# Optimization experiments

Measured on AMD Instinct MI355X. Metric: run time of the kernel, lower is better.

## Reference

```python
import jax, jax.numpy as jnp
import numpy as np

EPS = 0.1          # entropic regularization (init eps)
MAX_ITER = 20      # Sinkhorn iterations (init max_iter)
THRESH = 0.1       # convergence threshold on err (from torch source)
COS_EPS = 1e-8     # CosineSimilarity eps


def setup_inputs() -> dict:
    key = jax.random.key(0)
    kx, ky = jax.random.split(key)
    B, N, M, D = 4, 1024, 1024, 512
    x = jax.random.normal(kx, (B, N, D), dtype=jnp.float32)
    y = jax.random.normal(ky, (B, M, D), dtype=jnp.float32)
    nu = jnp.full((B, M), 1.0 / M, dtype=jnp.float32)  # target marginal
    return {"x": x, "y": y, "nu": nu}


def _cost_matrix(x, y):
    # C_ij = 1 - cos(x_i, y_j), with torch CosineSimilarity eps semantics
    dot = jnp.einsum("bnd,bmd->bnm", x, y)
    nx = jnp.linalg.norm(x, axis=-1)  # [B, N]
    ny = jnp.linalg.norm(y, axis=-1)  # [B, M]
    denom = jnp.maximum(nx[:, :, None] * ny[:, None, :], COS_EPS)
    return 1.0 - dot / denom  # [B, N, M]


def reference(x, y, nu):
    C = _cost_matrix(x, y)  # [B, N, M]
    B, N, _ = C.shape
    log_mu = jnp.log(jnp.full((B, N), 1.0 / N, dtype=C.dtype) + 1e-8)  # [B, N]
    log_nu = jnp.log(nu + 1e-8)  # [B, M]

    def Mmat(u, v):
        # M_ij = (-C_ij + u_i + v_j) / eps
        return (-C + u[:, :, None] + v[:, None, :]) / EPS

    def step(carry, _):
        u, v, done = carry
        u_new = EPS * (log_mu - jax.scipy.special.logsumexp(Mmat(u, v), axis=-1)) + u
        v_new = EPS * (log_nu - jax.scipy.special.logsumexp(Mmat(u_new, v), axis=-2)) + v
        err = jnp.abs(u_new - u).sum(-1).mean()
        # freeze updates after convergence (emulates the host-side break)
        u2 = jnp.where(done, u, u_new)
        v2 = jnp.where(done, v, v_new)
        return (u2, v2, done | (err < THRESH)), None

    u0 = jnp.zeros_like(log_mu)
    v0 = jnp.zeros_like(log_nu)
    (u, v, _), _ = jax.lax.scan(step, (u0, v0, jnp.array(False)), None, length=MAX_ITER)

    pi = jnp.exp(Mmat(u, v))  # transport plan [B, N, M]
    cost = jnp.sum(pi * C, axis=(-2, -1))  # [B]  (reduction='none')
    return cost
```

## Files before the change

kernel.cpp:

```cpp
#include <hip/hip_runtime.h>
#include <math.h>

#define EPS      0.1f
#define INV_EPS  10.0f
#define THRESH   0.1f
#define MAX_IT   20

#define BB 4
#define NN 1024
#define MM 1024
#define DD 512

#define MU_P (1.0f / 1024.0f + 1e-8f)

#define GBLK 128
#define TBLK 512

#define OFF_K    ((size_t)0)
#define OFF_XB   ((size_t)2097152)
#define OFF_YB   ((size_t)3145728)
#define OFF_NX   ((size_t)4194304)
#define OFF_NY   (OFF_NX + 4096)
#define OFF_NUP  (OFF_NY + 4096)
#define OFF_CS   (OFF_NUP + 4096)
#define OFF_FLG  (OFF_CS + 12288)

#define GLDA 40

typedef __bf16 bf16x8 __attribute__((ext_vector_type(8)));
typedef float f32x4 __attribute__((ext_vector_type(4)));
typedef unsigned long long u64;

__device__ __forceinline__ float wave_reduce_sum(float x) {
#pragma unroll
  for (int off = 32; off > 0; off >>= 1) x += __shfl_xor(x, off, 64);
  return x;
}

__device__ __forceinline__ uint pk2(float a, float b) {
  __bf16 ha = (__bf16)a, hb = (__bf16)b;
  return (uint)*(ushort*)&ha | ((uint)*(ushort*)&hb << 16);
}

__global__ void __launch_bounds__(256) prep_kernel(const float* __restrict__ x,
                                                   const float* __restrict__ y,
                                                   ushort* __restrict__ xb,
                                                   ushort* __restrict__ yb,
                                                   float* __restrict__ nx,
                                                   float* __restrict__ ny,
                                                   const float* __restrict__ nu,
                                                   float* nup, float* colsum,
                                                   int* flagsi, float* out) {
  const int tid = threadIdx.x;
  int gt = blockIdx.x * 256 + tid;
  if (gt < BB * MM) {
    nup[gt] = nu[gt] + 1e-8f;
    colsum[4096 + gt] = 0.f;
  }
  if (gt < 512) flagsi[gt] = 0;
  if (gt < BB) out[gt] = 0.f;

  const int w = tid >> 6, lane = tid & 63;
  const int r = blockIdx.x * 4 + w;
  const bool isx = (r < BB * NN);
  const float* src = isx ? (x + (size_t)r * DD)
                         : (y + (size_t)(r - BB * NN) * DD);
  ushort* dst = isx ? (xb + (size_t)r * DD)
                    : (yb + (size_t)(r - BB * NN) * DD);
  const float4* s4 = (const float4*)src;
  float4 a = s4[lane * 2];
  float4 b = s4[lane * 2 + 1];
  float ss = a.x * a.x + a.y * a.y + a.z * a.z + a.w * a.w +
             b.x * b.x + b.y * b.y + b.z * b.z + b.w * b.w;
  uint4 pk = make_uint4(pk2(a.x, a.y), pk2(a.z, a.w), pk2(b.x, b.y), pk2(b.z, b.w));
  *(uint4*)(dst + lane * 8) = pk;
  ss = wave_reduce_sum(ss);
  if (lane == 0) {
    float n = sqrtf(ss);
    if (isx) nx[r] = n; else ny[r - BB * NN] = n;
  }
}

__global__ void __launch_bounds__(256) gemm_kernel(const ushort* __restrict__ xb,
                                                   const ushort* __restrict__ yb,
                                                   const float* __restrict__ nxg,
                                                   const float* __restrict__ nyg,
                                                   ushort* __restrict__ K) {
  __shared__ ushort Ah[128 * GLDA];
  __shared__ ushort Bh[64 * GLDA];
  __shared__ float s_nx[128], s_ny[64];

  const int b = blockIdx.z;
  const int i0 = blockIdx.y * 128;
  const int j0 = blockIdx.x * 64;
  const int t = threadIdx.x;
  const int w = t >> 6, lane = t & 63;
  const int m16 = lane & 15, q = lane >> 4;
  const int wm = (w & 1) * 64, wn = (w >> 1) * 32;

  const int srA = t >> 1, soA = (t & 1) * 16;
  const int srB = t >> 2, soB = (t & 3) * 8;

  const ushort* xrow = xb + ((size_t)b * NN + i0 + srA) * DD + soA;
  const ushort* yrow = yb + ((size_t)b * MM + j0 + srB) * DD + soB;

  f32x4 acc[4][2];
#pragma unroll
  for (int mi = 0; mi < 4; ++mi)
#pragma unroll
    for (int ni = 0; ni < 2; ++ni) acc[mi][ni] = (f32x4)0.f;

  for (int k0 = 0; k0 < DD; k0 += 32) {
    uint4 av0 = *(const uint4*)(xrow + k0);
    uint4 av1 = *(const uint4*)(xrow + k0 + 8);
    uint4 bv0 = *(const uint4*)(yrow + k0);
    __syncthreads();
    *(uint4*)&Ah[srA * GLDA + soA] = av0;
    *(uint4*)&Ah[srA * GLDA + soA + 8] = av1;
    *(uint4*)&Bh[srB * GLDA + soB] = bv0;
    __syncthreads();

    bf16x8 ahf[4], bhf[2];
#pragma unroll
    for (int mi = 0; mi < 4; ++mi)
      ahf[mi] = *(const bf16x8*)&Ah[(wm + mi * 16 + m16) * GLDA + q * 8];
#pragma unroll
    for (int ni = 0; ni < 2; ++ni)
      bhf[ni] = *(const bf16x8*)&Bh[(wn + ni * 16 + m16) * GLDA + q * 8];
#pragma unroll
    for (int mi = 0; mi < 4; ++mi)
#pragma unroll
      for (int ni = 0; ni < 2; ++ni)
        acc[mi][ni] = __builtin_amdgcn_mfma_f32_16x16x32_bf16(ahf[mi], bhf[ni], acc[mi][ni], 0, 0, 0);
  }

  if (t < 128) s_nx[t] = nxg[b * NN + i0 + t];
  else if (t < 192) s_ny[t - 128] = nyg[b * MM + j0 + t - 128];
  __syncthreads();

#pragma unroll
  for (int mi = 0; mi < 4; ++mi)
#pragma unroll
    for (int ni = 0; ni < 2; ++ni)
#pragma unroll
      for (int r = 0; r < 4; ++r) {
        const int m = wm + mi * 16 + q * 4 + r;
        const int n = wn + ni * 16 + m16;
        float den = fmaxf(s_nx[m] * s_ny[n], 1e-8f);
        float cv = 1.0f - acc[mi][ni][r] / den;
        float kf = __expf(-cv * INV_EPS);
        __bf16 hb = (__bf16)kf;
        K[((size_t)b * NN + i0 + m) * MM + j0 + n] = *(ushort*)&hb;
      }
}

__device__ __forceinline__ void unpack8(uint4 k, float* kf) {
  kf[0] = __uint_as_float(k.x << 16);
  kf[1] = __uint_as_float(k.x & 0xffff0000u);
  kf[2] = __uint_as_float(k.y << 16);
  kf[3] = __uint_as_float(k.y & 0xffff0000u);
  kf[4] = __uint_as_float(k.z << 16);
  kf[5] = __uint_as_float(k.z & 0xffff0000u);
  kf[6] = __uint_as_float(k.w << 16);
  kf[7] = __uint_as_float(k.w & 0xffff0000u);
}

__global__ void __launch_bounds__(TBLK, 2) sinkhorn_kernel(
    const ushort* __restrict__ K, float* __restrict__ colsum,
    const float* __restrict__ nup, u64* __restrict__ flags,
    float* __restrict__ out) {
  const int tid = threadIdx.x;
  const int bid = blockIdx.x;
  const int lane = tid & 63;
  const int w = tid >> 6;
  const int b = bid >> 5;
  const int rbase = (bid & 31) * 32;

  __shared__ float swv[1024];
  __shared__ float spart[8][1024];
  __shared__ float s_red;
  __shared__ int s_conv;

  const float eps_log_mu = EPS * __logf(MU_P);
  float u_prev[4] = {0.f, 0.f, 0.f, 0.f};
  float wu_reg[4] = {0.f, 0.f, 0.f, 0.f};
  int T = 0;

  float kf[4][16];
#pragma unroll
  for (int rr = 0; rr < 4; ++rr) {
    const uint4* kp = (const uint4*)(K + ((size_t)b * NN + rbase + w * 4 + rr) * MM);
    uint4 k0 = kp[lane];
    uint4 k1 = kp[lane + 64];
    unpack8(k0, kf[rr]);
    unpack8(k1, kf[rr] + 8);
  }

  for (int it = 0; it < MAX_IT; ++it) {
    const int genv = it + 1;
    if (tid == 0) s_red = 0.f;
    if (it == 0) {
      swv[tid] = 1.f;
      swv[tid + 512] = 1.f;
    } else {
      const float* cs = colsum + (it % 3) * 4096 + b * MM;
      float c0 = __hip_atomic_load(cs + tid, __ATOMIC_RELAXED, __HIP_MEMORY_SCOPE_AGENT);
      float c1 = __hip_atomic_load(cs + tid + 512, __ATOMIC_RELAXED, __HIP_MEMORY_SCOPE_AGENT);
      swv[tid] = nup[b * MM + tid] / c0;
      swv[tid + 512] = nup[b * MM + tid + 512] / c1;
    }
    __syncthreads();

    float wvr[16];
    {
      const float4* wp = (const float4*)swv;
      *(float4*)&wvr[0] = wp[lane * 2];
      *(float4*)&wvr[4] = wp[lane * 2 + 1];
      *(float4*)&wvr[8] = wp[128 + lane * 2];
      *(float4*)&wvr[12] = wp[129 + lane * 2];
    }
    float creg[16];
#pragma unroll
    for (int t2 = 0; t2 < 16; ++t2) creg[t2] = 0.f;

    float werr = 0.f;
#pragma unroll
    for (int rr = 0; rr < 4; ++rr) {
      float s = 0.f;
#pragma unroll
      for (int t2 = 0; t2 < 16; ++t2) s = fmaf(kf[rr][t2], wvr[t2], s);
      s = wave_reduce_sum(s);
      float unv = eps_log_mu - EPS * __logf(s);
      werr += fabsf(unv - u_prev[rr]);
      u_prev[rr] = unv;
      float wu = MU_P / s;
      wu_reg[rr] = wu;
#pragma unroll
      for (int t2 = 0; t2 < 16; ++t2) creg[t2] = fmaf(wu, kf[rr][t2], creg[t2]);
    }
    if (lane == 0) atomicAdd(&s_red, werr);

    {
      float* pr = &spart[w][0];
      *(float4*)&pr[lane * 8] = *(float4*)&creg[0];
      *(float4*)&pr[lane * 8 + 4] = *(float4*)&creg[4];
      *(float4*)&pr[512 + lane * 8] = *(float4*)&creg[8];
      *(float4*)&pr[512 + lane * 8 + 4] = *(float4*)&creg[12];
    }
    __syncthreads();

    {
      float* csn = colsum + ((it + 1) % 3) * 4096 + b * MM;
      const int j0 = tid * 2;
      float s0 = 0.f, s1 = 0.f;
#pragma unroll
      for (int ww = 0; ww < 8; ++ww) {
        float2 p = *(const float2*)&spart[ww][j0];
        s0 += p.x;
        s1 += p.y;
      }
      unsafeAtomicAdd(&csn[j0], s0);
      unsafeAtomicAdd(&csn[j0 + 1], s1);
      if (tid < 32) {
        float* csz = colsum + ((it + 2) % 3) * 4096;
        __hip_atomic_store(&csz[bid * 32 + tid], 0.f, __ATOMIC_RELAXED, __HIP_MEMORY_SCOPE_AGENT);
      }
    }

    asm volatile("s_waitcnt vmcnt(0)" ::: "memory");
    __syncthreads();
    if (tid == 0) {
      u64 f = ((u64)(uint)genv << 32) | (u64)__float_as_uint(s_red);
      __hip_atomic_store(&flags[(genv & 1) * GBLK + bid], f, __ATOMIC_RELAXED, __HIP_MEMORY_SCOPE_AGENT);
    }
    if (tid < 64) {
      const u64* fl = flags + (genv & 1) * GBLK;
      u64 f0, f1;
      for (;;) {
        f0 = __hip_atomic_load(fl + tid, __ATOMIC_RELAXED, __HIP_MEMORY_SCOPE_AGENT);
        f1 = __hip_atomic_load(fl + tid + 64, __ATOMIC_RELAXED, __HIP_MEMORY_SCOPE_AGENT);
        if (__all(((f0 >> 32) >= (u64)genv) && ((f1 >> 32) >= (u64)genv))) break;
        __builtin_amdgcn_s_sleep(1);
      }
      float e = __uint_as_float((uint)f0) + __uint_as_float((uint)f1);
      e = wave_reduce_sum(e);
      if (tid == 0) s_conv = (e * (1.0f / (float)BB) < THRESH) ? 1 : 0;
    }
    __syncthreads();
    T = it;
    if (s_conv) break;
  }

  {
    const float* cs = colsum + ((T + 1) % 3) * 4096 + b * MM;
    float c0 = __hip_atomic_load(cs + tid, __ATOMIC_RELAXED, __HIP_MEMORY_SCOPE_AGENT);
    float c1 = __hip_atomic_load(cs + tid + 512, __ATOMIC_RELAXED, __HIP_MEMORY_SCOPE_AGENT);
    swv[tid] = nup[b * MM + tid] / c0;
    swv[tid + 512] = nup[b * MM + tid + 512] / c1;
  }
  if (tid == 0) s_red = 0.f;
  __syncthreads();

  float wvr[16];
  {
    const float4* wp = (const float4*)swv;
    *(float4*)&wvr[0] = wp[lane * 2];
    *(float4*)&wvr[4] = wp[lane * 2 + 1];
    *(float4*)&wvr[8] = wp[128 + lane * 2];
    *(float4*)&wvr[12] = wp[129 + lane * 2];
  }

  float wcost = 0.f;
#pragma unroll
  for (int rr = 0; rr < 4; ++rr) {
    float s = 0.f;
#pragma unroll
    for (int t2 = 0; t2 < 16; ++t2)
      s = fmaf(kf[rr][t2] * wvr[t2], -EPS * __logf(kf[rr][t2]), s);
    s = wave_reduce_sum(s) * wu_reg[rr];
    if (lane == 0) wcost += s;
  }
  if (lane == 0) atomicAdd(&s_red, wcost);
  __syncthreads();
  if (tid == 0) atomicAdd(out + b, s_red);
}

extern "C" void kernel_launch(void* const* d_in, const int* in_sizes, int n_in,
                              void* d_out, int out_size, void* d_ws, size_t ws_size,
                              hipStream_t stream) {
  const float* x = (const float*)d_in[0];
  const float* y = (const float*)d_in[1];
  const float* nu = (const float*)d_in[2];
  float* out = (float*)d_out;
  float* ws = (float*)d_ws;

  ushort* K = (ushort*)(ws + OFF_K);
  ushort* xb = (ushort*)(ws + OFF_XB);
  ushort* yb = (ushort*)(ws + OFF_YB);
  float* nx = ws + OFF_NX;
  float* ny = ws + OFF_NY;
  float* nup = ws + OFF_NUP;
  float* cs = ws + OFF_CS;
  u64* flg = (u64*)(ws + OFF_FLG);

  prep_kernel<<<2048, 256, 0, stream>>>(x, y, xb, yb, nx, ny, nu, nup, cs, (int*)flg, out);
  gemm_kernel<<<dim3(16, 8, 4), 256, 0, stream>>>(xb, yb, nx, ny, K);

  sinkhorn_kernel<<<GBLK, TBLK, 0, stream>>>(K, cs, nup, flg, out);
}
```

Before: 102.4 us.

## Fuse fp32-to-bf16 conversion and norm computation into GEMM, drop prep kernel

```diff
diff --git a/kernel.cpp b/kernel.cpp
--- a/kernel.cpp
+++ b/kernel.cpp
@@ -17,12 +17,7 @@
 #define TBLK 512
 
 #define OFF_K    ((size_t)0)
-#define OFF_XB   ((size_t)2097152)
-#define OFF_YB   ((size_t)3145728)
-#define OFF_NX   ((size_t)4194304)
-#define OFF_NY   (OFF_NX + 4096)
-#define OFF_NUP  (OFF_NY + 4096)
-#define OFF_CS   (OFF_NUP + 4096)
+#define OFF_CS   ((size_t)2097152)
 #define OFF_FLG  (OFF_CS + 12288)
 
 #define GLDA 40
@@ -42,50 +37,23 @@
   return (uint)*(ushort*)&ha | ((uint)*(ushort*)&hb << 16);
 }
 
-__global__ void __launch_bounds__(256) prep_kernel(const float* __restrict__ x,
+__device__ __forceinline__ void unpack8(uint4 k, float* kf) {
+  kf[0] = __uint_as_float(k.x << 16);
+  kf[1] = __uint_as_float(k.x & 0xffff0000u);
+  kf[2] = __uint_as_float(k.y << 16);
+  kf[3] = __uint_as_float(k.y & 0xffff0000u);
+  kf[4] = __uint_as_float(k.z << 16);
+  kf[5] = __uint_as_float(k.z & 0xffff0000u);
+  kf[6] = __uint_as_float(k.w << 16);
+  kf[7] = __uint_as_float(k.w & 0xffff0000u);
+}
+
+__global__ void __launch_bounds__(256) gemm_kernel(const float* __restrict__ x,
                                                    const float* __restrict__ y,
-                                                   ushort* __restrict__ xb,
-                                                   ushort* __restrict__ yb,
-                                                   float* __restrict__ nx,
-                                                   float* __restrict__ ny,
-                                                   const float* __restrict__ nu,
-                                                   float* nup, float* colsum,
-                                                   int* flagsi, float* out) {
-  const int tid = threadIdx.x;
-  int gt = blockIdx.x * 256 + tid;
-  if (gt < BB * MM) {
-    nup[gt] = nu[gt] + 1e-8f;
-    colsum[4096 + gt] = 0.f;
-  }
-  if (gt < 512) flagsi[gt] = 0;
-  if (gt < BB) out[gt] = 0.f;
-
-  const int w = tid >> 6, lane = tid & 63;
-  const int r = blockIdx.x * 4 + w;
-  const bool isx = (r < BB * NN);
-  const float* src = isx ? (x + (size_t)r * DD)
-                         : (y + (size_t)(r - BB * NN) * DD);
-  ushort* dst = isx ? (xb + (size_t)r * DD)
-                    : (yb + (size_t)(r - BB * NN) * DD);
-  const float4* s4 = (const float4*)src;
-  float4 a = s4[lane * 2];
-  float4 b = s4[lane * 2 + 1];
-  float ss = a.x * a.x + a.y * a.y + a.z * a.z + a.w * a.w +
-             b.x * b.x + b.y * b.y + b.z * b.z + b.w * b.w;
-  uint4 pk = make_uint4(pk2(a.x, a.y), pk2(a.z, a.w), pk2(b.x, b.y), pk2(b.z, b.w));
-  *(uint4*)(dst + lane * 8) = pk;
-  ss = wave_reduce_sum(ss);
-  if (lane == 0) {
-    float n = sqrtf(ss);
-    if (isx) nx[r] = n; else ny[r - BB * NN] = n;
-  }
-}
-
-__global__ void __launch_bounds__(256) gemm_kernel(const ushort* __restrict__ xb,
-                                                   const ushort* __restrict__ yb,
-                                                   const float* __restrict__ nxg,
-                                                   const float* __restrict__ nyg,
-                                                   ushort* __restrict__ K) {
+                                                   ushort* __restrict__ K,
+                                                   float* __restrict__ colsum,
+                                                   int* __restrict__ flagsi,
+                                                   float* __restrict__ out) {
   __shared__ ushort Ah[128 * GLDA];
   __shared__ ushort Bh[64 * GLDA];
   __shared__ float s_nx[128], s_ny[64];
@@ -98,11 +66,19 @@
   const int m16 = lane & 15, q = lane >> 4;
   const int wm = (w & 1) * 64, wn = (w >> 1) * 32;
 
+  {
+    const int bid = blockIdx.x + (blockIdx.y << 4) + (blockIdx.z << 7);
+    const int gt = bid * 256 + t;
+    if (gt < BB * MM) colsum[4096 + gt] = 0.f;
+    if (gt < 512) flagsi[gt] = 0;
+    if (gt < BB) out[gt] = 0.f;
+  }
+
   const int srA = t >> 1, soA = (t & 1) * 16;
   const int srB = t >> 2, soB = (t & 3) * 8;
 
-  const ushort* xrow = xb + ((size_t)b * NN + i0 + srA) * DD + soA;
-  const ushort* yrow = yb + ((size_t)b * MM + j0 + srB) * DD + soB;
+  const float* xrow = x + ((size_t)b * NN + i0 + srA) * DD + soA;
+  const float* yrow = y + ((size_t)b * MM + j0 + srB) * DD + soB;
 
   f32x4 acc[4][2];
 #pragma unroll
@@ -110,14 +86,27 @@
 #pragma unroll
     for (int ni = 0; ni < 2; ++ni) acc[mi][ni] = (f32x4)0.f;
 
+  float ssA = 0.f, ssB = 0.f;
   for (int k0 = 0; k0 < DD; k0 += 32) {
-    uint4 av0 = *(const uint4*)(xrow + k0);
-    uint4 av1 = *(const uint4*)(xrow + k0 + 8);
-    uint4 bv0 = *(const uint4*)(yrow + k0);
-    __syncthreads();
-    *(uint4*)&Ah[srA * GLDA + soA] = av0;
-    *(uint4*)&Ah[srA * GLDA + soA + 8] = av1;
-    *(uint4*)&Bh[srB * GLDA + soB] = bv0;
+    float4 a0 = *(const float4*)(xrow + k0);
+    float4 a1 = *(const float4*)(xrow + k0 + 4);
+    float4 a2 = *(const float4*)(xrow + k0 + 8);
+    float4 a3 = *(const float4*)(xrow + k0 + 12);
+    float4 b0 = *(const float4*)(yrow + k0);
+    float4 b1 = *(const float4*)(yrow + k0 + 4);
+    ssA += a0.x * a0.x + a0.y * a0.y + a0.z * a0.z + a0.w * a0.w +
+           a1.x * a1.x + a1.y * a1.y + a1.z * a1.z + a1.w * a1.w +
+           a2.x * a2.x + a2.y * a2.y + a2.z * a2.z + a2.w * a2.w +
+           a3.x * a3.x + a3.y * a3.y + a3.z * a3.z + a3.w * a3.w;
+    ssB += b0.x * b0.x + b0.y * b0.y + b0.z * b0.z + b0.w * b0.w +
+           b1.x * b1.x + b1.y * b1.y + b1.z * b1.z + b1.w * b1.w;
+    uint4 pa0 = make_uint4(pk2(a0.x, a0.y), pk2(a0.z, a0.w), pk2(a1.x, a1.y), pk2(a1.z, a1.w));
+    uint4 pa1 = make_uint4(pk2(a2.x, a2.y), pk2(a2.z, a2.w), pk2(a3.x, a3.y), pk2(a3.z, a3.w));
+    uint4 pb0 = make_uint4(pk2(b0.x, b0.y), pk2(b0.z, b0.w), pk2(b1.x, b1.y), pk2(b1.z, b1.w));
+    __syncthreads();
+    *(uint4*)&Ah[srA * GLDA + soA] = pa0;
+    *(uint4*)&Ah[srA * GLDA + soA + 8] = pa1;
+    *(uint4*)&Bh[srB * GLDA + soB] = pb0;
     __syncthreads();
 
     bf16x8 ahf[4], bhf[2];
@@ -134,8 +123,11 @@
         acc[mi][ni] = __builtin_amdgcn_mfma_f32_16x16x32_bf16(ahf[mi], bhf[ni], acc[mi][ni], 0, 0, 0);
   }
 
-  if (t < 128) s_nx[t] = nxg[b * NN + i0 + t];
-  else if (t < 192) s_ny[t - 128] = nyg[b * MM + j0 + t - 128];
+  ssA += __shfl_xor(ssA, 1, 64);
+  ssB += __shfl_xor(ssB, 1, 64);
+  ssB += __shfl_xor(ssB, 2, 64);
+  if ((t & 1) == 0) s_nx[srA] = sqrtf(ssA);
+  if ((t & 3) == 0) s_ny[srB] = sqrtf(ssB);
   __syncthreads();
 
 #pragma unroll
@@ -154,20 +146,9 @@
       }
 }
 
-__device__ __forceinline__ void unpack8(uint4 k, float* kf) {
-  kf[0] = __uint_as_float(k.x << 16);
-  kf[1] = __uint_as_float(k.x & 0xffff0000u);
-  kf[2] = __uint_as_float(k.y << 16);
-  kf[3] = __uint_as_float(k.y & 0xffff0000u);
-  kf[4] = __uint_as_float(k.z << 16);
-  kf[5] = __uint_as_float(k.z & 0xffff0000u);
-  kf[6] = __uint_as_float(k.w << 16);
-  kf[7] = __uint_as_float(k.w & 0xffff0000u);
-}
-
 __global__ void __launch_bounds__(TBLK, 2) sinkhorn_kernel(
     const ushort* __restrict__ K, float* __restrict__ colsum,
-    const float* __restrict__ nup, u64* __restrict__ flags,
+    const float* __restrict__ nu, u64* __restrict__ flags,
     float* __restrict__ out) {
   const int tid = threadIdx.x;
   const int bid = blockIdx.x;
@@ -206,8 +187,8 @@
       const float* cs = colsum + (it % 3) * 4096 + b * MM;
       float c0 = __hip_atomic_load(cs + tid, __ATOMIC_RELAXED, __HIP_MEMORY_SCOPE_AGENT);
       float c1 = __hip_atomic_load(cs + tid + 512, __ATOMIC_RELAXED, __HIP_MEMORY_SCOPE_AGENT);
-      swv[tid] = nup[b * MM + tid] / c0;
-      swv[tid + 512] = nup[b * MM + tid + 512] / c1;
+      swv[tid] = (nu[b * MM + tid] + 1e-8f) / c0;
+      swv[tid + 512] = (nu[b * MM + tid + 512] + 1e-8f) / c1;
     }
     __syncthreads();
 
@@ -295,8 +276,8 @@
     const float* cs = colsum + ((T + 1) % 3) * 4096 + b * MM;
     float c0 = __hip_atomic_load(cs + tid, __ATOMIC_RELAXED, __HIP_MEMORY_SCOPE_AGENT);
     float c1 = __hip_atomic_load(cs + tid + 512, __ATOMIC_RELAXED, __HIP_MEMORY_SCOPE_AGENT);
-    swv[tid] = nup[b * MM + tid] / c0;
-    swv[tid + 512] = nup[b * MM + tid + 512] / c1;
+    swv[tid] = (nu[b * MM + tid] + 1e-8f) / c0;
+    swv[tid + 512] = (nu[b * MM + tid + 512] + 1e-8f) / c1;
   }
   if (tid == 0) s_red = 0.f;
   __syncthreads();
@@ -335,16 +316,10 @@
   float* ws = (float*)d_ws;
 
   ushort* K = (ushort*)(ws + OFF_K);
-  ushort* xb = (ushort*)(ws + OFF_XB);
-  ushort* yb = (ushort*)(ws + OFF_YB);
-  float* nx = ws + OFF_NX;
-  float* ny = ws + OFF_NY;
-  float* nup = ws + OFF_NUP;
   float* cs = ws + OFF_CS;
   u64* flg = (u64*)(ws + OFF_FLG);
 
-  prep_kernel<<<2048, 256, 0, stream>>>(x, y, xb, yb, nx, ny, nu, nup, cs, (int*)flg, out);
-  gemm_kernel<<<dim3(16, 8, 4), 256, 0, stream>>>(xb, yb, nx, ny, K);
-
-  sinkhorn_kernel<<<GBLK, TBLK, 0, stream>>>(K, cs, nup, flg, out);
-}
+  gemm_kernel<<<dim3(16, 8, 4), 256, 0, stream>>>(x, y, K, cs, (int*)flg, out);
+
+  sinkhorn_kernel<<<GBLK, TBLK, 0, stream>>>(K, cs, nu, flg, out);
+}
```

New measurement: 105.0 us. 1.03x slower.
